# Kernel tuning notes

Measured on AMD Instinct MI355X. Metric: run time of the kernel, lower is better.

The kernel has to match this reference:

```python
import jax, jax.numpy as jnp
import numpy as np
import math

B, SQ, SK, D, H = 2, 2048, 2048, 1024, 16
DH = D // H
EPS = 1e-5

def _ln(x, g, b):
    m = jnp.mean(x, axis=-1, keepdims=True)
    v = jnp.mean(jnp.square(x - m), axis=-1, keepdims=True)
    return (x - m) / jnp.sqrt(v + EPS) * g + b

def setup_inputs() -> dict:
    key = jax.random.key(0)
    ks = jax.random.split(key, 8)
    xav = math.sqrt(6.0 / (D + D))  # xavier_uniform for square [D,D] weights
    inp = {
        'Q': jax.random.normal(ks[0], (B, SQ, D), dtype=jnp.float32),
        'K': jax.random.normal(ks[1], (B, SK, D), dtype=jnp.float32),
        'pad_mask': jax.random.randint(ks[2], (B, SK), 0, 2, dtype=jnp.int32),
        'Wq': jax.random.uniform(ks[3], (D, D), jnp.float32, -xav, xav),
        'Wk': jax.random.uniform(ks[4], (D, D), jnp.float32, -xav, xav),
        'Wv': jax.random.uniform(ks[5], (D, D), jnp.float32, -xav, xav),
        'Wo': jax.random.uniform(ks[6], (D, D), jnp.float32, -xav, xav),
        'bq': jnp.zeros((D,), jnp.float32),
        'bk': jnp.zeros((D,), jnp.float32),
        'bv': jnp.zeros((D,), jnp.float32),
        'bo': jnp.zeros((D,), jnp.float32),
        'ln_q_g': jnp.ones((D,), jnp.float32),  'ln_q_b': jnp.zeros((D,), jnp.float32),
        'ln_kv_g': jnp.ones((D,), jnp.float32), 'ln_kv_b': jnp.zeros((D,), jnp.float32),
        'ln_f_g': jnp.ones((D,), jnp.float32),  'ln_f_b': jnp.zeros((D,), jnp.float32),
    }
    return inp

def reference(Q, K, pad_mask, Wq, Wk, Wv, Wo, bq, bk, bv, bo,
              ln_q_g, ln_q_b, ln_kv_g, ln_kv_b, ln_f_g, ln_f_b):
    Q_ = _ln(Q, ln_q_g, ln_q_b)
    K_ = _ln(K, ln_kv_g, ln_kv_b)
    # projections (PyTorch Linear: x @ W.T + b)
    Q1 = (Q_ @ Wq.T + bq).reshape(B, SQ, H, DH)
    K1 = (K_ @ Wk.T + bk).reshape(B, SK, H, DH)
    V1 = (K_ @ Wv.T + bv).reshape(B, SK, H, DH)
    # note: scaling uses sqrt(dim_V), NOT sqrt(head_dim), per source
    score = jnp.einsum('bqhd,bkhd->bhqk', Q1, K1) / math.sqrt(D)
    m = pad_mask[:, None, None, :]  # [B,1,1,SK]
    score = jnp.where(m == 0, jnp.float32(-1e12), score)
    A = jax.nn.softmax(score, axis=-1)
    A = A * m.astype(A.dtype)  # second mask application after softmax
    O1 = jnp.einsum('bhqk,bkhd->bqhd', A, V1).reshape(B, SQ, D)
    O2 = jax.nn.relu(Q_ @ Wo.T + bo)
    return _ln(Q + O1 + O2, ln_f_g, ln_f_b)
```

## Files before the change

kernel.cpp:

```cpp
#include <hip/hip_runtime.h>
#include <stdint.h>

#define NB 2
#define NSQ 2048
#define NSK 2048
#define ND 1024
#define NH 16
#define NDH 64

typedef unsigned short u16;
typedef unsigned int u32;
typedef __bf16 bf16x8_t __attribute__((ext_vector_type(8)));
typedef float f32x4_t __attribute__((ext_vector_type(4)));
typedef u32 u32x4_t __attribute__((ext_vector_type(4)));
typedef short s16x4 __attribute__((ext_vector_type(4)));
typedef u32 u32x2_t __attribute__((ext_vector_type(2)));

#define AS1 __attribute__((address_space(1)))
#define AS3 __attribute__((address_space(3)))

__device__ __forceinline__ float bf2f(u16 u) {
    union { float f; u32 i; } v; v.i = ((u32)u) << 16; return v.f;
}
__device__ __forceinline__ u16 f2bf(float x) {
    union { float f; u32 i; } v; v.f = x;
    u32 r = v.i + 0x7fffu + ((v.i >> 16) & 1u);
    return (u16)(r >> 16);
}
__device__ __forceinline__ u32 fbits(float x) {
    union { float f; u32 i; } v; v.f = x; return v.i;
}
__device__ __forceinline__ float fexp2(float x) {
#if __has_builtin(__builtin_amdgcn_exp2f)
    return __builtin_amdgcn_exp2f(x);
#else
    return exp2f(x);
#endif
}
__device__ __forceinline__ f32x4_t mfma16(s16x4 a, s16x4 b, f32x4_t c) {
#if __has_builtin(__builtin_amdgcn_mfma_f32_16x16x16bf16_1k)
    return __builtin_amdgcn_mfma_f32_16x16x16bf16_1k(a, b, c, 0, 0, 0);
#else
    asm("v_mfma_f32_16x16x16_bf16 %0, %1, %2, %0" : "+v"(c) : "v"(a), "v"(b));
    return c;
#endif
}

__global__ __launch_bounds__(256) void detect_kernel(
    const u16* __restrict__ Q, int* __restrict__ flag)
{
    __shared__ int s;
    if (threadIdx.x == 0) s = 0;
    __syncthreads();
    uint2 x = ((const uint2*)Q)[threadIdx.x];
    u16 a0 = x.x & 0xffff, a1 = x.x >> 16, a2 = x.y & 0xffff, a3 = x.y >> 16;
    bool big = (((a0 >> 7) & 0xff) >= 0x8D) || (((a1 >> 7) & 0xff) >= 0x8D) ||
               (((a2 >> 7) & 0xff) >= 0x8D) || (((a3 >> 7) & 0xff) >= 0x8D);
    if (big) s = 1;
    __syncthreads();
    if (threadIdx.x == 0) *flag = s;
}

__global__ __launch_bounds__(256) void cvt_params_kernel(
    const int* __restrict__ flag,
    const void* __restrict__ Wq, const void* __restrict__ Wk,
    const void* __restrict__ Wv, const void* __restrict__ Wo,
    const void* __restrict__ vbq, const void* __restrict__ vbk,
    const void* __restrict__ vbv, const void* __restrict__ vbo,
    const void* __restrict__ g0, const void* __restrict__ b0,
    const void* __restrict__ g1, const void* __restrict__ b1,
    const void* __restrict__ g2, const void* __restrict__ b2,
    u16* __restrict__ Wc, u16* __restrict__ Vc)
{
    int blk = blockIdx.x;
    int t = threadIdx.x;
    const void* src;
    u16* dst;
    size_t srcoff;
    if (blk < 4096) {
        int w = blk >> 10;
        src = (w == 0) ? Wq : (w == 1) ? Wk : (w == 2) ? Wv : Wo;
        srcoff = (size_t)(blk & 1023) * 1024;
        dst = Wc + (size_t)w * 1024 * 1024 + srcoff;
    } else {
        int v = blk - 4096;
        src = (v == 0) ? vbq : (v == 1) ? vbk : (v == 2) ? vbv : (v == 3) ? vbo :
              (v == 4) ? g0  : (v == 5) ? b0  : (v == 6) ? g1  : (v == 7) ? b1 :
              (v == 8) ? g2  : b2;
        srcoff = 0;
        dst = Vc + (size_t)v * 1024;
    }
    u32 lo, hi;
    if (*flag) {
        float4 x = ((const float4*)src)[srcoff / 4 + t];
        lo = (u32)f2bf(x.x) | ((u32)f2bf(x.y) << 16);
        hi = (u32)f2bf(x.z) | ((u32)f2bf(x.w) << 16);
    } else {
        uint2 x = ((const uint2*)src)[srcoff / 4 + t];
        lo = x.x; hi = x.y;
    }
    uint2 o; o.x = lo; o.y = hi;
    ((uint2*)dst)[t] = o;
}

__global__ __launch_bounds__(256) void idx_kernel(
    const int* __restrict__ mask, int* __restrict__ idx, int* __restrict__ cnt)
{
    int b = blockIdx.x;
    const int* m = mask + b * NSK;
    int t = threadIdx.x;
    int loc[8]; int s = 0;
#pragma unroll
    for (int i = 0; i < 8; ++i) { loc[i] = (m[t * 8 + i] != 0); s += loc[i]; }
    __shared__ int ps[256];
    ps[t] = s;
    __syncthreads();
    for (int off = 1; off < 256; off <<= 1) {
        int v = (t >= off) ? ps[t - off] : 0;
        __syncthreads();
        ps[t] += v;
        __syncthreads();
    }
    int run = ps[t] - s;
#pragma unroll
    for (int i = 0; i < 8; ++i)
        if (loc[i]) idx[b * NSK + run++] = t * 8 + i;
    if (t == 255) cnt[b] = ps[255];
}

__global__ __launch_bounds__(256) void ln_in_kernel(
    const int* __restrict__ flag,
    const void* __restrict__ Q, const void* __restrict__ K,
    const u16* __restrict__ Vc,
    u16* __restrict__ Qn, u16* __restrict__ Kn)
{
    int row = blockIdx.x;
    const void* x; const u16 *g, *bb; u16* y;
    size_t roff;
    if (row < NB * NSQ) {
        x = Q; roff = (size_t)row * ND;
        g = Vc + 4 * 1024; bb = Vc + 5 * 1024;
        y = Qn + roff;
    } else {
        int r2 = row - NB * NSQ;
        x = K; roff = (size_t)r2 * ND;
        g = Vc + 6 * 1024; bb = Vc + 7 * 1024;
        y = Kn + roff;
    }
    int t = threadIdx.x;
    float v0, v1, v2, v3;
    if (*flag) {
        float4 xv = ((const float4*)x)[roff / 4 + t];
        v0 = xv.x; v1 = xv.y; v2 = xv.z; v3 = xv.w;
    } else {
        uint2 ux = ((const uint2*)x)[roff / 4 + t];
        v0 = bf2f(ux.x & 0xffff); v1 = bf2f(ux.x >> 16);
        v2 = bf2f(ux.y & 0xffff); v3 = bf2f(ux.y >> 16);
    }
    float s1 = v0 + v1 + v2 + v3;
    float s2 = v0*v0 + v1*v1 + v2*v2 + v3*v3;
#pragma unroll
    for (int off = 32; off >= 1; off >>= 1) {
        s1 += __shfl_xor(s1, off);
        s2 += __shfl_xor(s2, off);
    }
    __shared__ float r1[4], r2[4];
    int wave = t >> 6;
    if ((t & 63) == 0) { r1[wave] = s1; r2[wave] = s2; }
    __syncthreads();
    float t1 = r1[0] + r1[1] + r1[2] + r1[3];
    float t2 = r2[0] + r2[1] + r2[2] + r2[3];
    float mean = t1 * (1.0f / ND);
    float var  = t2 * (1.0f / ND) - mean * mean;
    float rstd = rsqrtf(var + 1e-5f);
    uint2 ug = ((const uint2*)g)[t];
    uint2 ub = ((const uint2*)bb)[t];
    float y0 = (v0 - mean) * rstd * bf2f(ug.x & 0xffff) + bf2f(ub.x & 0xffff);
    float y1 = (v1 - mean) * rstd * bf2f(ug.x >> 16)    + bf2f(ub.x >> 16);
    float y2 = (v2 - mean) * rstd * bf2f(ug.y & 0xffff) + bf2f(ub.y & 0xffff);
    float y3 = (v3 - mean) * rstd * bf2f(ug.y >> 16)    + bf2f(ub.y >> 16);
    uint2 o;
    o.x = (u32)f2bf(y0) | ((u32)f2bf(y1) << 16);
    o.y = (u32)f2bf(y2) | ((u32)f2bf(y3) << 16);
    ((uint2*)y)[t] = o;
}

__global__ __launch_bounds__(512, 2) void gemm4_kernel(
    const u16* __restrict__ Qn, const u16* __restrict__ Kn,
    const u16* __restrict__ Wc, const u16* __restrict__ Vc,
    u16* __restrict__ Q1, u16* __restrict__ K1, u16* __restrict__ V1,
    u16* __restrict__ R)
{
    int lin = blockIdx.x + 16 * blockIdx.y + 64 * blockIdx.z;
    int u   = (lin & 7) * 32 + (lin >> 3);
    int bx  = u & 15;
    int by  = (u >> 4) & 3;
    int z   = u >> 6;

    const u16* X    = (z == 0 || z == 3) ? Qn : Kn;
    const u16* W    = Wc + (size_t)z * 1024 * 1024;
    const u16* bias = Vc + (size_t)z * 1024;

    __shared__ u16 sm[4][2][256 * 32];

    int tid  = threadIdx.x;
    int wave = tid >> 6, lane = tid & 63;
    int wm = wave >> 2, wn = wave & 3;
    int quad = lane >> 4, l4 = lane & 15;
    int m0 = bx * 256;
    int n0 = by * 256;

    int srow   = wave * 16 + (lane >> 2);
    int schunk = (lane & 3) ^ ((srow >> 1) & 3);
    const u16* gA = X + (size_t)(m0 + srow) * ND + schunk * 8;
    const u16* gB = W + (size_t)(n0 + srow) * ND + schunk * 8;

#define STAGE_A(t_) do { int s_ = (t_) & 3; \
    __builtin_amdgcn_global_load_lds((const AS1 u32*)(gA + (t_) * 32), \
        (AS3 u32*)(&sm[s_][0][wave * 512]), 16, 0, 0); \
    __builtin_amdgcn_global_load_lds((const AS1 u32*)(gA + (t_) * 32 + (size_t)128 * ND), \
        (AS3 u32*)(&sm[s_][0][4096 + wave * 512]), 16, 0, 0); \
} while (0)
#define STAGE_B(t_) do { int s_ = (t_) & 3; \
    __builtin_amdgcn_global_load_lds((const AS1 u32*)(gB + (t_) * 32), \
        (AS3 u32*)(&sm[s_][1][wave * 512]), 16, 0, 0); \
    __builtin_amdgcn_global_load_lds((const AS1 u32*)(gB + (t_) * 32 + (size_t)128 * ND), \
        (AS3 u32*)(&sm[s_][1][4096 + wave * 512]), 16, 0, 0); \
} while (0)

    int fch   = (quad ^ ((l4 >> 1) & 3)) * 8;
    int aoffb = (wm * 128 + l4) * 32 + fch;
    int boffb = (wn * 64  + l4) * 32 + fch;

    f32x4_t acc[8][4];
#pragma unroll
    for (int i = 0; i < 8; ++i)
#pragma unroll
        for (int j = 0; j < 4; ++j)
            acc[i][j] = (f32x4_t){0.f, 0.f, 0.f, 0.f};

    STAGE_A(0); STAGE_B(0);
    STAGE_A(1); STAGE_B(1);
    STAGE_A(2); STAGE_B(2);
    asm volatile("s_waitcnt vmcnt(8)" ::: "memory");
    __builtin_amdgcn_s_barrier();
    __builtin_amdgcn_sched_barrier(0);

    for (int t = 0; t < 32; ++t) {
        const u16* a = &sm[t & 3][0][0];
        const u16* b = &sm[t & 3][1][0];
        bf16x8_t bf[4], af[4], ah[4];

#pragma unroll
        for (int nf = 0; nf < 4; ++nf)
            bf[nf] = *(const bf16x8_t*)(b + boffb + nf * 512);
#pragma unroll
        for (int mf = 0; mf < 4; ++mf)
            af[mf] = *(const bf16x8_t*)(a + aoffb + mf * 512);
#pragma unroll
        for (int mf = 0; mf < 4; ++mf)
            ah[mf] = *(const bf16x8_t*)(a + aoffb + (mf + 4) * 512);

        if (t < 29) { STAGE_A(t + 3); STAGE_B(t + 3); }

        __builtin_amdgcn_s_setprio(1);
#pragma unroll
        for (int mf = 0; mf < 4; ++mf)
#pragma unroll
            for (int nf = 0; nf < 4; ++nf)
                acc[mf][nf] = __builtin_amdgcn_mfma_f32_16x16x32_bf16(
                    af[mf], bf[nf], acc[mf][nf], 0, 0, 0);
#pragma unroll
        for (int mf = 0; mf < 4; ++mf)
#pragma unroll
            for (int nf = 0; nf < 4; ++nf)
                acc[mf + 4][nf] = __builtin_amdgcn_mfma_f32_16x16x32_bf16(
                    ah[mf], bf[nf], acc[mf + 4][nf], 0, 0, 0);
        __builtin_amdgcn_s_setprio(0);

        if (t < 29)       asm volatile("s_waitcnt vmcnt(8)" ::: "memory");
        else if (t == 29) asm volatile("s_waitcnt vmcnt(4)" ::: "memory");
        else if (t == 30) asm volatile("s_waitcnt vmcnt(0)" ::: "memory");
        __builtin_amdgcn_s_barrier();
        __builtin_amdgcn_sched_barrier(0);
    }
#undef STAGE_A
#undef STAGE_B

    u16* outp = (z == 0) ? Q1 : (z == 1) ? K1 : (z == 2) ? V1 : R;
    float bv_[4];
#pragma unroll
    for (int nf = 0; nf < 4; ++nf)
        bv_[nf] = bf2f(bias[n0 + wn * 64 + nf * 16 + l4]);
#pragma unroll
    for (int mf = 0; mf < 8; ++mf) {
#pragma unroll
        for (int r = 0; r < 4; ++r) {
            int m = m0 + wm * 128 + mf * 16 + quad * 4 + r;
#pragma unroll
            for (int nf = 0; nf < 4; ++nf) {
                int n = n0 + wn * 64 + nf * 16 + l4;
                float val = acc[mf][nf][r] + bv_[nf];
                if (z == 0) val *= 0.045105964f;
                if (z == 3) val = fmaxf(val, 0.f);
                outp[(size_t)m * ND + n] = f2bf(val);
            }
        }
    }
}

__global__ __launch_bounds__(256) void gather_k_kernel(
    const u16* __restrict__ K1, const int* __restrict__ idx,
    const int* __restrict__ cnt, u16* __restrict__ Kc)
{
    int b = blockIdx.y;
    int c = cnt[b];
    int cPad = (c + 63) & ~63;
    int jb = blockIdx.x * 16;
    if (jb >= cPad) return;
    int t = threadIdx.x;
    int row = t >> 4;
    int seg = t & 15;
    int j = jb + row;
    if (j >= cPad) return;
    bool z = (j >= c);
    const u16* src = z ? (const u16*)0
        : K1 + ((size_t)b * NSK + idx[(size_t)b * NSK + j]) * ND;
    u16* dst = Kc + ((size_t)b * NSK + j) * ND;
#pragma unroll
    for (int i = 0; i < 8; ++i) {
        int off = (seg * 8 + i) * 8;
        uint4 v = z ? (uint4){0, 0, 0, 0} : *(const uint4*)(src + off);
        *(uint4*)(dst + off) = v;
    }
}

__global__ __launch_bounds__(256) void gather_vt_kernel(
    const u16* __restrict__ V1, const int* __restrict__ idx,
    const int* __restrict__ cnt, u16* __restrict__ Vct)
{
    int kb = blockIdx.x;
    int h  = blockIdx.y;
    int b  = blockIdx.z;
    int c = cnt[b];
    int cPad = (c + 63) & ~63;
    if (kb * 64 >= cPad) return;
    __shared__ u16 sT[64 * 72];
    int tid = threadIdx.x;
    {
        int row = tid >> 3, seg = tid & 7;
        int j1 = kb * 64 + row, j2 = j1 + 32;
        uint4 v1 = {0, 0, 0, 0}, v2 = {0, 0, 0, 0};
        if (j1 < c) v1 = *(const uint4*)(V1 +
            ((size_t)b * NSK + idx[(size_t)b * NSK + j1]) * ND + h * NDH + seg * 8);
        if (j2 < c) v2 = *(const uint4*)(V1 +
            ((size_t)b * NSK + idx[(size_t)b * NSK + j2]) * ND + h * NDH + seg * 8);
        *(uint4*)(sT + row * 72 + seg * 8) = v1;
        *(uint4*)(sT + (row + 32) * 72 + seg * 8) = v2;
    }
    __syncthreads();
    int d = tid >> 2, sg = tid & 3;
    u16 buf[16];
#pragma unroll
    for (int i = 0; i < 8; ++i) buf[i]     = sT[(sg * 8 + i) * 72 + d];
#pragma unroll
    for (int i = 0; i < 8; ++i) buf[8 + i] = sT[((sg + 4) * 8 + i) * 72 + d];
    u16* go = Vct + ((size_t)(b * NH + h) * NDH + d) * NSK + kb * 64;
    *(uint4*)(go + sg * 8)       = *(uint4*)buf;
    *(uint4*)(go + (sg + 4) * 8) = *(uint4*)(buf + 8);
}

__global__ __launch_bounds__(256, 4) void attn_kernel(
    const u16* __restrict__ Q1, const u16* __restrict__ Kc,
    const u16* __restrict__ Vct, const int* __restrict__ cnt,
    u16* __restrict__ R)
{
    int q0 = blockIdx.x * 64;
    int h  = blockIdx.y;
    int b  = blockIdx.z;

    __shared__ u16 sK[2][64 * 64];
    __shared__ u16 sV[2][64 * 64];

    int tid  = threadIdx.x;
    int wave = tid >> 6, lane = tid & 63;
    int quad = lane >> 4, l4 = lane & 15;
    int lk = lane >> 3, ls = lane & 7;
    int gseg = ls ^ lk;

    int c  = cnt[b];
    int nt = (c + 63) >> 6;

    bf16x8_t qf[2];
    {
        const u16* qp = Q1 + (size_t)(b * NSQ + q0 + wave * 16 + l4) * ND + h * NDH;
        qf[0] = *(const bf16x8_t*)(qp + quad * 8);
        qf[1] = *(const bf16x8_t*)(qp + 32 + quad * 8);
    }

    const u16* kbase = Kc + (size_t)b * NSK * ND + h * NDH;
    const u16* vbase = Vct + (size_t)(b * NH + h) * NDH * NSK;

    const u16* gk0 = kbase + (size_t)(wave * 16 + lk) * ND + gseg * 8;
    const u16* gk1 = gk0 + (size_t)8 * ND;
    const u16* gv0 = vbase + (size_t)(wave * 16 + lk) * NSK + gseg * 8;
    const u16* gv1 = gv0 + (size_t)8 * NSK;

    int fragOff[2];
#pragma unroll
    for (int kk = 0; kk < 2; ++kk)
        fragOff[kk] = l4 * 64 + (((kk * 4 + quad) ^ (l4 & 7)) * 8);

    int v4off[4];
#pragma unroll
    for (int tm = 0; tm < 4; ++tm)
        v4off[tm] = l4 * 64 + (((2 * tm + (quad >> 1)) ^ (l4 & 7)) * 8)
                  + (quad & 1) * 4;

    float l_run = 0.f;
    f32x4_t acc_o[4];
#pragma unroll
    for (int T = 0; T < 4; ++T) acc_o[T] = (f32x4_t){0.f, 0.f, 0.f, 0.f};

    if (nt > 0) {
        __builtin_amdgcn_global_load_lds((const AS1 u32*)gk0,
            (AS3 u32*)(&sK[0][(wave * 16) * 64]), 16, 0, 0);
        __builtin_amdgcn_global_load_lds((const AS1 u32*)gk1,
            (AS3 u32*)(&sK[0][(wave * 16 + 8) * 64]), 16, 0, 0);
        __builtin_amdgcn_global_load_lds((const AS1 u32*)gv0,
            (AS3 u32*)(&sV[0][(wave * 16) * 64]), 16, 0, 0);
        __builtin_amdgcn_global_load_lds((const AS1 u32*)gv1,
            (AS3 u32*)(&sV[0][(wave * 16 + 8) * 64]), 16, 0, 0);
        gk0 += (size_t)64 * ND; gk1 += (size_t)64 * ND;
        gv0 += 64; gv1 += 64;

        for (int kb = 0; kb < nt; ++kb) {
            __syncthreads();

            if (kb + 1 < nt) {
                int bi = (kb + 1) & 1;
                __builtin_amdgcn_global_load_lds((const AS1 u32*)gk0,
                    (AS3 u32*)(&sK[bi][(wave * 16) * 64]), 16, 0, 0);
                __builtin_amdgcn_global_load_lds((const AS1 u32*)gk1,
                    (AS3 u32*)(&sK[bi][(wave * 16 + 8) * 64]), 16, 0, 0);
                __builtin_amdgcn_global_load_lds((const AS1 u32*)gv0,
                    (AS3 u32*)(&sV[bi][(wave * 16) * 64]), 16, 0, 0);
                __builtin_amdgcn_global_load_lds((const AS1 u32*)gv1,
                    (AS3 u32*)(&sV[bi][(wave * 16 + 8) * 64]), 16, 0, 0);
                gk0 += (size_t)64 * ND; gk1 += (size_t)64 * ND;
                gv0 += 64; gv1 += 64;
            }

            const u16* kt = sK[kb & 1];
            const u16* vt = sV[kb & 1];

            f32x4_t accs[4];
            if (kb == nt - 1) {
#pragma unroll
                for (int tm = 0; tm < 4; ++tm) {
                    int key = kb * 64 + tm * 16 + quad * 4;
#pragma unroll
                    for (int r = 0; r < 4; ++r)
                        accs[tm][r] = (key + r < c) ? 0.f : -1e9f;
                }
            } else {
#pragma unroll
                for (int tm = 0; tm < 4; ++tm)
                    accs[tm] = (f32x4_t){0.f, 0.f, 0.f, 0.f};
            }
#pragma unroll
            for (int kk = 0; kk < 2; ++kk)
#pragma unroll
                for (int tm = 0; tm < 4; ++tm) {
                    bf16x8_t kf = *(const bf16x8_t*)(kt + tm * 1024 + fragOff[kk]);
                    accs[tm] = __builtin_amdgcn_mfma_f32_16x16x32_bf16(
                        kf, qf[kk], accs[tm], 0, 0, 0);
                }

            float lsum = 0.f;
#pragma unroll
            for (int tm = 0; tm < 4; ++tm) {
                float p0 = fexp2(accs[tm][0]);
                float p1 = fexp2(accs[tm][1]);
                float p2 = fexp2(accs[tm][2]);
                float p3 = fexp2(accs[tm][3]);
                lsum += (p0 + p1) + (p2 + p3);
                u32 lo = __builtin_amdgcn_perm(fbits(p1), fbits(p0), 0x07060302);
                u32 hi = __builtin_amdgcn_perm(fbits(p3), fbits(p2), 0x07060302);
                s16x4 pf = __builtin_bit_cast(s16x4, (u32x2_t){lo, hi});
#pragma unroll
                for (int T = 0; T < 4; ++T) {
                    s16x4 vf = *(const s16x4*)(vt + T * 1024 + v4off[tm]);
                    acc_o[T] = mfma16(vf, pf, acc_o[T]);
                }
            }
            lsum += __shfl_xor(lsum, 16);
            lsum += __shfl_xor(lsum, 32);
            l_run += lsum;
        }
    }

    float inv = l_run > 0.f ? 1.f / l_run : 0.f;
    u16* rp = R + (size_t)(b * NSQ + q0 + wave * 16 + l4) * ND + h * NDH;
#pragma unroll
    for (int T = 0; T < 4; ++T) {
        u16* p = rp + T * 16 + quad * 4;
        uint2 o2 = *(const uint2*)p;
        float e0 = acc_o[T][0] * inv + bf2f(o2.x & 0xffff);
        float e1 = acc_o[T][1] * inv + bf2f(o2.x >> 16);
        float e2 = acc_o[T][2] * inv + bf2f(o2.y & 0xffff);
        float e3 = acc_o[T][3] * inv + bf2f(o2.y >> 16);
        uint2 on;
        on.x = (u32)f2bf(e0) | ((u32)f2bf(e1) << 16);
        on.y = (u32)f2bf(e2) | ((u32)f2bf(e3) << 16);
        *(uint2*)p = on;
    }
}

__global__ __launch_bounds__(256) void ln_out_kernel(
    const int* __restrict__ flag,
    const void* __restrict__ Q, const u16* __restrict__ R,
    const u16* __restrict__ Vc, void* __restrict__ out)
{
    int row = blockIdx.x;
    size_t roff = (size_t)row * ND;
    int t = threadIdx.x;
    int f = *flag;
    float v0, v1, v2, v3;
    uint2 ur = ((const uint2*)(R + roff))[t];
    if (f) {
        float4 xq = ((const float4*)Q)[roff / 4 + t];
        v0 = xq.x; v1 = xq.y; v2 = xq.z; v3 = xq.w;
    } else {
        uint2 uq = ((const uint2*)Q)[roff / 4 + t];
        v0 = bf2f(uq.x & 0xffff); v1 = bf2f(uq.x >> 16);
        v2 = bf2f(uq.y & 0xffff); v3 = bf2f(uq.y >> 16);
    }
    v0 += bf2f(ur.x & 0xffff); v1 += bf2f(ur.x >> 16);
    v2 += bf2f(ur.y & 0xffff); v3 += bf2f(ur.y >> 16);
    float s1 = v0 + v1 + v2 + v3;
    float s2 = v0*v0 + v1*v1 + v2*v2 + v3*v3;
#pragma unroll
    for (int off = 32; off >= 1; off >>= 1) {
        s1 += __shfl_xor(s1, off);
        s2 += __shfl_xor(s2, off);
    }
    __shared__ float r1[4], r2[4];
    int wave = t >> 6;
    if ((t & 63) == 0) { r1[wave] = s1; r2[wave] = s2; }
    __syncthreads();
    float t1 = r1[0] + r1[1] + r1[2] + r1[3];
    float t2 = r2[0] + r2[1] + r2[2] + r2[3];
    float mean = t1 * (1.0f / ND);
    float var  = t2 * (1.0f / ND) - mean * mean;
    float rstd = rsqrtf(var + 1e-5f);
    const u16* g  = Vc + 8 * 1024;
    const u16* bb = Vc + 9 * 1024;
    uint2 ug = ((const uint2*)g)[t];
    uint2 ub = ((const uint2*)bb)[t];
    float y0 = (v0 - mean) * rstd * bf2f(ug.x & 0xffff) + bf2f(ub.x & 0xffff);
    float y1 = (v1 - mean) * rstd * bf2f(ug.x >> 16)    + bf2f(ub.x >> 16);
    float y2 = (v2 - mean) * rstd * bf2f(ug.y & 0xffff) + bf2f(ub.y & 0xffff);
    float y3 = (v3 - mean) * rstd * bf2f(ug.y >> 16)    + bf2f(ub.y >> 16);
    if (f) {
        float4 o; o.x = y0; o.y = y1; o.z = y2; o.w = y3;
        ((float4*)out)[roff / 4 + t] = o;
    } else {
        uint2 o;
        o.x = (u32)f2bf(y0) | ((u32)f2bf(y1) << 16);
        o.y = (u32)f2bf(y2) | ((u32)f2bf(y3) << 16);
        ((uint2*)out)[roff / 4 + t] = o;
    }
}

extern "C" void kernel_launch(void* const* d_in, const int* in_sizes, int n_in,
                              void* d_out, int out_size, void* d_ws, size_t ws_size,
                              hipStream_t stream) {
    const void* Q        = d_in[0];
    const void* K        = d_in[1];
    const int* pad_mask  = (const int*)d_in[2];

    const size_t NEL = (size_t)NB * NSQ * ND;
    int* flag = (int*)d_ws;
    int* cnt  = flag + 1;
    int* idx  = flag + 4;
    u16* base = (u16*)(idx + 4096);
    u16* Qn  = base;
    u16* Kn  = Qn + NEL;
    u16* Q1  = Kn + NEL;
    u16* K1  = Q1 + NEL;
    u16* V1  = K1 + NEL;
    u16* R   = V1 + NEL;
    u16* Wc  = R + NEL;
    u16* Vc  = Wc + (size_t)4 * 1024 * 1024;
    u16* Kc  = Qn;
    u16* Vct = Kn;

    detect_kernel<<<dim3(1), dim3(256), 0, stream>>>((const u16*)Q, flag);

    cvt_params_kernel<<<dim3(4106), dim3(256), 0, stream>>>(
        flag, d_in[3], d_in[4], d_in[5], d_in[6],
        d_in[7], d_in[8], d_in[9], d_in[10],
        d_in[11], d_in[12], d_in[13], d_in[14], d_in[15], d_in[16],
        Wc, Vc);

    idx_kernel<<<dim3(NB), dim3(256), 0, stream>>>(pad_mask, idx, cnt);

    ln_in_kernel<<<dim3(2 * NB * NSQ), dim3(256), 0, stream>>>(
        flag, Q, K, Vc, Qn, Kn);

    gemm4_kernel<<<dim3(16, 4, 4), dim3(512), 0, stream>>>(
        Qn, Kn, Wc, Vc, Q1, K1, V1, R);

    gather_k_kernel<<<dim3(128, NB), dim3(256), 0, stream>>>(K1, idx, cnt, Kc);

    gather_vt_kernel<<<dim3(32, NH, NB), dim3(256), 0, stream>>>(V1, idx, cnt, Vct);

    attn_kernel<<<dim3(NSQ / 64, NH, NB), dim3(256), 0, stream>>>(
        Q1, Kc, Vct, cnt, R);

    ln_out_kernel<<<dim3(NB * NSQ), dim3(256), 0, stream>>>(
        flag, Q, R, Vc, d_out);
}
```

Before: 225.6 us.

## Merge prep kernels into one launch and fuse K/V gathers

Replaces the separate detect, parameter-convert, index-scan and input-layernorm kernels with one prep_kernel whose block ranges do each job. The dtype flag is now recomputed in every block with a wave-level __any, so no launch has to wait for it. The K gather and the V-transpose gather are also merged into a single launch. The aim is fewer kernel launches and fewer serial dependencies, at the cost of one small redundant read of Q per block and a more heterogeneous grid.

```diff
diff --git a/kernel.cpp b/kernel.cpp
--- a/kernel.cpp
+++ b/kernel.cpp
@@ -45,24 +45,19 @@
     return c;
 #endif
 }
-
-__global__ __launch_bounds__(256) void detect_kernel(
-    const u16* __restrict__ Q, int* __restrict__ flag)
-{
-    __shared__ int s;
-    if (threadIdx.x == 0) s = 0;
-    __syncthreads();
-    uint2 x = ((const uint2*)Q)[threadIdx.x];
+__device__ __forceinline__ int detect_f32(const u16* __restrict__ Q) {
+    uint2 x = ((const uint2*)Q)[threadIdx.x & 63];
     u16 a0 = x.x & 0xffff, a1 = x.x >> 16, a2 = x.y & 0xffff, a3 = x.y >> 16;
     bool big = (((a0 >> 7) & 0xff) >= 0x8D) || (((a1 >> 7) & 0xff) >= 0x8D) ||
                (((a2 >> 7) & 0xff) >= 0x8D) || (((a3 >> 7) & 0xff) >= 0x8D);
-    if (big) s = 1;
-    __syncthreads();
-    if (threadIdx.x == 0) *flag = s;
-}
-
-__global__ __launch_bounds__(256) void cvt_params_kernel(
-    const int* __restrict__ flag,
+    return __any(big);
+}
+
+#define PREP_LN   (2 * NB * NSQ)
+#define PREP_CVT  4106
+__global__ __launch_bounds__(256) void prep_kernel(
+    const void* __restrict__ Q, const void* __restrict__ K,
+    const int* __restrict__ pad_mask,
     const void* __restrict__ Wq, const void* __restrict__ Wk,
     const void* __restrict__ Wv, const void* __restrict__ Wo,
     const void* __restrict__ vbq, const void* __restrict__ vbk,
@@ -70,119 +65,122 @@
     const void* __restrict__ g0, const void* __restrict__ b0,
     const void* __restrict__ g1, const void* __restrict__ b1,
     const void* __restrict__ g2, const void* __restrict__ b2,
-    u16* __restrict__ Wc, u16* __restrict__ Vc)
-{
-    int blk = blockIdx.x;
-    int t = threadIdx.x;
-    const void* src;
-    u16* dst;
-    size_t srcoff;
-    if (blk < 4096) {
-        int w = blk >> 10;
-        src = (w == 0) ? Wq : (w == 1) ? Wk : (w == 2) ? Wv : Wo;
-        srcoff = (size_t)(blk & 1023) * 1024;
-        dst = Wc + (size_t)w * 1024 * 1024 + srcoff;
-    } else {
-        int v = blk - 4096;
-        src = (v == 0) ? vbq : (v == 1) ? vbk : (v == 2) ? vbv : (v == 3) ? vbo :
-              (v == 4) ? g0  : (v == 5) ? b0  : (v == 6) ? g1  : (v == 7) ? b1 :
-              (v == 8) ? g2  : b2;
-        srcoff = 0;
-        dst = Vc + (size_t)v * 1024;
-    }
-    u32 lo, hi;
-    if (*flag) {
-        float4 x = ((const float4*)src)[srcoff / 4 + t];
-        lo = (u32)f2bf(x.x) | ((u32)f2bf(x.y) << 16);
-        hi = (u32)f2bf(x.z) | ((u32)f2bf(x.w) << 16);
-    } else {
-        uint2 x = ((const uint2*)src)[srcoff / 4 + t];
-        lo = x.x; hi = x.y;
-    }
-    uint2 o; o.x = lo; o.y = hi;
-    ((uint2*)dst)[t] = o;
-}
-
-__global__ __launch_bounds__(256) void idx_kernel(
-    const int* __restrict__ mask, int* __restrict__ idx, int* __restrict__ cnt)
-{
-    int b = blockIdx.x;
-    const int* m = mask + b * NSK;
-    int t = threadIdx.x;
-    int loc[8]; int s = 0;
-#pragma unroll
-    for (int i = 0; i < 8; ++i) { loc[i] = (m[t * 8 + i] != 0); s += loc[i]; }
-    __shared__ int ps[256];
-    ps[t] = s;
-    __syncthreads();
-    for (int off = 1; off < 256; off <<= 1) {
-        int v = (t >= off) ? ps[t - off] : 0;
-        __syncthreads();
-        ps[t] += v;
-        __syncthreads();
-    }
-    int run = ps[t] - s;
-#pragma unroll
-    for (int i = 0; i < 8; ++i)
-        if (loc[i]) idx[b * NSK + run++] = t * 8 + i;
-    if (t == 255) cnt[b] = ps[255];
-}
-
-__global__ __launch_bounds__(256) void ln_in_kernel(
-    const int* __restrict__ flag,
-    const void* __restrict__ Q, const void* __restrict__ K,
-    const u16* __restrict__ Vc,
+    u16* __restrict__ Wc, u16* __restrict__ Vc,
+    int* __restrict__ idx, int* __restrict__ cnt,
     u16* __restrict__ Qn, u16* __restrict__ Kn)
 {
-    int row = blockIdx.x;
-    const void* x; const u16 *g, *bb; u16* y;
-    size_t roff;
-    if (row < NB * NSQ) {
-        x = Q; roff = (size_t)row * ND;
-        g = Vc + 4 * 1024; bb = Vc + 5 * 1024;
-        y = Qn + roff;
+    int bx = blockIdx.x;
+    int t  = threadIdx.x;
+
+    if (bx < PREP_LN) {
+        int flag = detect_f32((const u16*)Q);
+        int row = bx;
+        const void* x; const void *gv, *bv; u16* y;
+        size_t roff;
+        if (row < NB * NSQ) {
+            x = Q; roff = (size_t)row * ND;
+            gv = g0; bv = b0;
+            y = Qn + roff;
+        } else {
+            int r2 = row - NB * NSQ;
+            x = K; roff = (size_t)r2 * ND;
+            gv = g1; bv = b1;
+            y = Kn + roff;
+        }
+        float v0, v1, v2, v3, gg0, gg1, gg2, gg3, bb0, bb1, bb2, bb3;
+        if (flag) {
+            float4 xv = ((const float4*)x)[roff / 4 + t];
+            v0 = xv.x; v1 = xv.y; v2 = xv.z; v3 = xv.w;
+            float4 G = ((const float4*)gv)[t];
+            float4 Bv = ((const float4*)bv)[t];
+            gg0 = G.x; gg1 = G.y; gg2 = G.z; gg3 = G.w;
+            bb0 = Bv.x; bb1 = Bv.y; bb2 = Bv.z; bb3 = Bv.w;
+        } else {
+            uint2 ux = ((const uint2*)x)[roff / 4 + t];
+            v0 = bf2f(ux.x & 0xffff); v1 = bf2f(ux.x >> 16);
+            v2 = bf2f(ux.y & 0xffff); v3 = bf2f(ux.y >> 16);
+            uint2 G = ((const uint2*)gv)[t];
+            uint2 Bv = ((const uint2*)bv)[t];
+            gg0 = bf2f(G.x & 0xffff); gg1 = bf2f(G.x >> 16);
+            gg2 = bf2f(G.y & 0xffff); gg3 = bf2f(G.y >> 16);
+            bb0 = bf2f(Bv.x & 0xffff); bb1 = bf2f(Bv.x >> 16);
+            bb2 = bf2f(Bv.y & 0xffff); bb3 = bf2f(Bv.y >> 16);
+        }
+        float s1 = v0 + v1 + v2 + v3;
+        float s2 = v0*v0 + v1*v1 + v2*v2 + v3*v3;
+#pragma unroll
+        for (int off = 32; off >= 1; off >>= 1) {
+            s1 += __shfl_xor(s1, off);
+            s2 += __shfl_xor(s2, off);
+        }
+        __shared__ float r1[4], r2[4];
+        int wave = t >> 6;
+        if ((t & 63) == 0) { r1[wave] = s1; r2[wave] = s2; }
+        __syncthreads();
+        float t1 = r1[0] + r1[1] + r1[2] + r1[3];
+        float t2 = r2[0] + r2[1] + r2[2] + r2[3];
+        float mean = t1 * (1.0f / ND);
+        float var  = t2 * (1.0f / ND) - mean * mean;
+        float rstd = rsqrtf(var + 1e-5f);
+        float y0 = (v0 - mean) * rstd * gg0 + bb0;
+        float y1 = (v1 - mean) * rstd * gg1 + bb1;
+        float y2 = (v2 - mean) * rstd * gg2 + bb2;
+        float y3 = (v3 - mean) * rstd * gg3 + bb3;
+        uint2 o;
+        o.x = (u32)f2bf(y0) | ((u32)f2bf(y1) << 16);
+        o.y = (u32)f2bf(y2) | ((u32)f2bf(y3) << 16);
+        ((uint2*)y)[t] = o;
+    } else if (bx < PREP_LN + PREP_CVT) {
+        int flag = detect_f32((const u16*)Q);
+        int blk = bx - PREP_LN;
+        const void* src;
+        u16* dst;
+        size_t srcoff;
+        if (blk < 4096) {
+            int w = blk >> 10;
+            src = (w == 0) ? Wq : (w == 1) ? Wk : (w == 2) ? Wv : Wo;
+            srcoff = (size_t)(blk & 1023) * 1024;
+            dst = Wc + (size_t)w * 1024 * 1024 + srcoff;
+        } else {
+            int v = blk - 4096;
+            src = (v == 0) ? vbq : (v == 1) ? vbk : (v == 2) ? vbv : (v == 3) ? vbo :
+                  (v == 4) ? g0  : (v == 5) ? b0  : (v == 6) ? g1  : (v == 7) ? b1 :
+                  (v == 8) ? g2  : b2;
+            srcoff = 0;
+            dst = Vc + (size_t)v * 1024;
+        }
+        u32 lo, hi;
+        if (flag) {
+            float4 x = ((const float4*)src)[srcoff / 4 + t];
+            lo = (u32)f2bf(x.x) | ((u32)f2bf(x.y) << 16);
+            hi = (u32)f2bf(x.z) | ((u32)f2bf(x.w) << 16);
+        } else {
+            uint2 x = ((const uint2*)src)[srcoff / 4 + t];
+            lo = x.x; hi = x.y;
+        }
+        uint2 o; o.x = lo; o.y = hi;
+        ((uint2*)dst)[t] = o;
     } else {
-        int r2 = row - NB * NSQ;
-        x = K; roff = (size_t)r2 * ND;
-        g = Vc + 6 * 1024; bb = Vc + 7 * 1024;
-        y = Kn + roff;
-    }
-    int t = threadIdx.x;
-    float v0, v1, v2, v3;
-    if (*flag) {
-        float4 xv = ((const float4*)x)[roff / 4 + t];
-        v0 = xv.x; v1 = xv.y; v2 = xv.z; v3 = xv.w;
-    } else {
-        uint2 ux = ((const uint2*)x)[roff / 4 + t];
-        v0 = bf2f(ux.x & 0xffff); v1 = bf2f(ux.x >> 16);
-        v2 = bf2f(ux.y & 0xffff); v3 = bf2f(ux.y >> 16);
-    }
-    float s1 = v0 + v1 + v2 + v3;
-    float s2 = v0*v0 + v1*v1 + v2*v2 + v3*v3;
-#pragma unroll
-    for (int off = 32; off >= 1; off >>= 1) {
-        s1 += __shfl_xor(s1, off);
-        s2 += __shfl_xor(s2, off);
-    }
-    __shared__ float r1[4], r2[4];
-    int wave = t >> 6;
-    if ((t & 63) == 0) { r1[wave] = s1; r2[wave] = s2; }
-    __syncthreads();
-    float t1 = r1[0] + r1[1] + r1[2] + r1[3];
-    float t2 = r2[0] + r2[1] + r2[2] + r2[3];
-    float mean = t1 * (1.0f / ND);
-    float var  = t2 * (1.0f / ND) - mean * mean;
-    float rstd = rsqrtf(var + 1e-5f);
-    uint2 ug = ((const uint2*)g)[t];
-    uint2 ub = ((const uint2*)bb)[t];
-    float y0 = (v0 - mean) * rstd * bf2f(ug.x & 0xffff) + bf2f(ub.x & 0xffff);
-    float y1 = (v1 - mean) * rstd * bf2f(ug.x >> 16)    + bf2f(ub.x >> 16);
-    float y2 = (v2 - mean) * rstd * bf2f(ug.y & 0xffff) + bf2f(ub.y & 0xffff);
-    float y3 = (v3 - mean) * rstd * bf2f(ug.y >> 16)    + bf2f(ub.y >> 16);
-    uint2 o;
-    o.x = (u32)f2bf(y0) | ((u32)f2bf(y1) << 16);
-    o.y = (u32)f2bf(y2) | ((u32)f2bf(y3) << 16);
-    ((uint2*)y)[t] = o;
+        int b = bx - (PREP_LN + PREP_CVT);
+        const int* m = pad_mask + b * NSK;
+        int loc[8]; int s = 0;
+#pragma unroll
+        for (int i = 0; i < 8; ++i) { loc[i] = (m[t * 8 + i] != 0); s += loc[i]; }
+        __shared__ int ps[256];
+        ps[t] = s;
+        __syncthreads();
+        for (int off = 1; off < 256; off <<= 1) {
+            int v = (t >= off) ? ps[t - off] : 0;
+            __syncthreads();
+            ps[t] += v;
+            __syncthreads();
+        }
+        int run = ps[t] - s;
+#pragma unroll
+        for (int i = 0; i < 8; ++i)
+            if (loc[i]) idx[b * NSK + run++] = t * 8 + i;
+        if (t == 255) cnt[b] = ps[255];
+    }
 }
 
 __global__ __launch_bounds__(512, 2) void gemm4_kernel(
@@ -309,65 +307,61 @@
     }
 }
 
-__global__ __launch_bounds__(256) void gather_k_kernel(
-    const u16* __restrict__ K1, const int* __restrict__ idx,
-    const int* __restrict__ cnt, u16* __restrict__ Kc)
+__global__ __launch_bounds__(256) void gather_kernel(
+    const u16* __restrict__ K1, const u16* __restrict__ V1,
+    const int* __restrict__ idx, const int* __restrict__ cnt,
+    u16* __restrict__ Kc, u16* __restrict__ Vct)
 {
     int b = blockIdx.y;
     int c = cnt[b];
     int cPad = (c + 63) & ~63;
-    int jb = blockIdx.x * 16;
-    if (jb >= cPad) return;
-    int t = threadIdx.x;
-    int row = t >> 4;
-    int seg = t & 15;
-    int j = jb + row;
-    if (j >= cPad) return;
-    bool z = (j >= c);
-    const u16* src = z ? (const u16*)0
-        : K1 + ((size_t)b * NSK + idx[(size_t)b * NSK + j]) * ND;
-    u16* dst = Kc + ((size_t)b * NSK + j) * ND;
-#pragma unroll
-    for (int i = 0; i < 8; ++i) {
-        int off = (seg * 8 + i) * 8;
-        uint4 v = z ? (uint4){0, 0, 0, 0} : *(const uint4*)(src + off);
-        *(uint4*)(dst + off) = v;
-    }
-}
-
-__global__ __launch_bounds__(256) void gather_vt_kernel(
-    const u16* __restrict__ V1, const int* __restrict__ idx,
-    const int* __restrict__ cnt, u16* __restrict__ Vct)
-{
-    int kb = blockIdx.x;
-    int h  = blockIdx.y;
-    int b  = blockIdx.z;
-    int c = cnt[b];
-    int cPad = (c + 63) & ~63;
-    if (kb * 64 >= cPad) return;
-    __shared__ u16 sT[64 * 72];
     int tid = threadIdx.x;
-    {
-        int row = tid >> 3, seg = tid & 7;
-        int j1 = kb * 64 + row, j2 = j1 + 32;
-        uint4 v1 = {0, 0, 0, 0}, v2 = {0, 0, 0, 0};
-        if (j1 < c) v1 = *(const uint4*)(V1 +
-            ((size_t)b * NSK + idx[(size_t)b * NSK + j1]) * ND + h * NDH + seg * 8);
-        if (j2 < c) v2 = *(const uint4*)(V1 +
-            ((size_t)b * NSK + idx[(size_t)b * NSK + j2]) * ND + h * NDH + seg * 8);
-        *(uint4*)(sT + row * 72 + seg * 8) = v1;
-        *(uint4*)(sT + (row + 32) * 72 + seg * 8) = v2;
-    }
-    __syncthreads();
-    int d = tid >> 2, sg = tid & 3;
-    u16 buf[16];
-#pragma unroll
-    for (int i = 0; i < 8; ++i) buf[i]     = sT[(sg * 8 + i) * 72 + d];
-#pragma unroll
-    for (int i = 0; i < 8; ++i) buf[8 + i] = sT[((sg + 4) * 8 + i) * 72 + d];
-    u16* go = Vct + ((size_t)(b * NH + h) * NDH + d) * NSK + kb * 64;
-    *(uint4*)(go + sg * 8)       = *(uint4*)buf;
-    *(uint4*)(go + (sg + 4) * 8) = *(uint4*)(buf + 8);
+
+    if (blockIdx.x < 128) {
+        int jb = blockIdx.x * 16;
+        if (jb >= cPad) return;
+        int row = tid >> 4;
+        int seg = tid & 15;
+        int j = jb + row;
+        if (j >= cPad) return;
+        bool z = (j >= c);
+        const u16* src = z ? (const u16*)0
+            : K1 + ((size_t)b * NSK + idx[(size_t)b * NSK + j]) * ND;
+        u16* dst = Kc + ((size_t)b * NSK + j) * ND;
+#pragma unroll
+        for (int i = 0; i < 8; ++i) {
+            int off = (seg * 8 + i) * 8;
+            uint4 v = z ? (uint4){0, 0, 0, 0} : *(const uint4*)(src + off);
+            *(uint4*)(dst + off) = v;
+        }
+    } else {
+        int lin = blockIdx.x - 128;
+        int kb = lin & 31;
+        int h  = lin >> 5;
+        if (kb * 64 >= cPad) return;
+        __shared__ u16 sT[64 * 72];
+        {
+            int row = tid >> 3, seg = tid & 7;
+            int j1 = kb * 64 + row, j2 = j1 + 32;
+            uint4 v1 = {0, 0, 0, 0}, v2 = {0, 0, 0, 0};
+            if (j1 < c) v1 = *(const uint4*)(V1 +
+                ((size_t)b * NSK + idx[(size_t)b * NSK + j1]) * ND + h * NDH + seg * 8);
+            if (j2 < c) v2 = *(const uint4*)(V1 +
+                ((size_t)b * NSK + idx[(size_t)b * NSK + j2]) * ND + h * NDH + seg * 8);
+            *(uint4*)(sT + row * 72 + seg * 8) = v1;
+            *(uint4*)(sT + (row + 32) * 72 + seg * 8) = v2;
+        }
+        __syncthreads();
+        int d = tid >> 2, sg = tid & 3;
+        u16 buf[16];
+#pragma unroll
+        for (int i = 0; i < 8; ++i) buf[i]     = sT[(sg * 8 + i) * 72 + d];
+#pragma unroll
+        for (int i = 0; i < 8; ++i) buf[8 + i] = sT[((sg + 4) * 8 + i) * 72 + d];
+        u16* go = Vct + ((size_t)(b * NH + h) * NDH + d) * NSK + kb * 64;
+        *(uint4*)(go + sg * 8)       = *(uint4*)buf;
+        *(uint4*)(go + (sg + 4) * 8) = *(uint4*)(buf + 8);
+    }
 }
 
 __global__ __launch_bounds__(256, 4) void attn_kernel(
@@ -518,14 +512,13 @@
 }
 
 __global__ __launch_bounds__(256) void ln_out_kernel(
-    const int* __restrict__ flag,
     const void* __restrict__ Q, const u16* __restrict__ R,
     const u16* __restrict__ Vc, void* __restrict__ out)
 {
     int row = blockIdx.x;
     size_t roff = (size_t)row * ND;
     int t = threadIdx.x;
-    int f = *flag;
+    int f = detect_f32((const u16*)Q);
     float v0, v1, v2, v3;
     uint2 ur = ((const uint2*)(R + roff))[t];
     if (f) {
@@ -596,29 +589,22 @@
     u16* Kc  = Qn;
     u16* Vct = Kn;
 
-    detect_kernel<<<dim3(1), dim3(256), 0, stream>>>((const u16*)Q, flag);
-
-    cvt_params_kernel<<<dim3(4106), dim3(256), 0, stream>>>(
-        flag, d_in[3], d_in[4], d_in[5], d_in[6],
+    prep_kernel<<<dim3(PREP_LN + PREP_CVT + NB), dim3(256), 0, stream>>>(
+        Q, K, pad_mask,
+        d_in[3], d_in[4], d_in[5], d_in[6],
         d_in[7], d_in[8], d_in[9], d_in[10],
         d_in[11], d_in[12], d_in[13], d_in[14], d_in[15], d_in[16],
-        Wc, Vc);
-
-    idx_kernel<<<dim3(NB), dim3(256), 0, stream>>>(pad_mask, idx, cnt);
-
-    ln_in_kernel<<<dim3(2 * NB * NSQ), dim3(256), 0, stream>>>(
-        flag, Q, K, Vc, Qn, Kn);
+        Wc, Vc, idx, cnt, Qn, Kn);
 
     gemm4_kernel<<<dim3(16, 4, 4), dim3(512), 0, stream>>>(
         Qn, Kn, Wc, Vc, Q1, K1, V1, R);
 
-    gather_k_kernel<<<dim3(128, NB), dim3(256), 0, stream>>>(K1, idx, cnt, Kc);
-
-    gather_vt_kernel<<<dim3(32, NH, NB), dim3(256), 0, stream>>>(V1, idx, cnt, Vct);
+    gather_kernel<<<dim3(128 + 32 * NH, NB), dim3(256), 0, stream>>>(
+        K1, V1, idx, cnt, Kc, Vct);
 
     attn_kernel<<<dim3(NSQ / 64, NH, NB), dim3(256), 0, stream>>>(
         Q1, Kc, Vct, cnt, R);
 
     ln_out_kernel<<<dim3(NB * NSQ), dim3(256), 0, stream>>>(
-        flag, Q, R, Vc, d_out);
-}
+        Q, R, Vc, d_out);
+}
```

Result: faster. 213.7 us (-5.3%).
